# Optimization experiments

Measured on AMD Instinct MI355X. Metric: run time of the kernel, lower is better.

## Reference

```python
import jax, jax.numpy as jnp
import numpy as np

FEATURE_DIM = 128
NUM_EDGES = 640000
NUM_NODES = 40000


def setup_inputs() -> dict:
    key = jax.random.key(0)
    ks = jax.random.split(key, 10)
    d = FEATURE_DIM
    scale = 1.0 / np.sqrt(d)
    inp = {
        "messages": jax.random.normal(ks[0], (NUM_EDGES, d), dtype=jnp.float32),
        "receivers": jax.random.randint(ks[1], (NUM_EDGES,), 0, NUM_NODES, dtype=jnp.int32),
        "num_segments": NUM_NODES,
        "Wk": jax.random.normal(ks[2], (d, d), dtype=jnp.float32) * scale,
        "bk": jnp.zeros((d,), dtype=jnp.float32),
        "Wv": jax.random.normal(ks[3], (d, d), dtype=jnp.float32) * scale,
        "bv": jnp.zeros((d,), dtype=jnp.float32),
        "Wq": jax.random.normal(ks[4], (d, d), dtype=jnp.float32) * scale,
        "bq": jnp.zeros((d,), dtype=jnp.float32),
        "Wo": jax.random.normal(ks[5], (d, d), dtype=jnp.float32) * scale,
        "bo": jnp.zeros((d,), dtype=jnp.float32),
    }
    return inp


def reference(messages, receivers, num_segments, Wk, bk, Wv, bv, Wq, bq, Wo, bo):
    d = messages.shape[-1]
    # per-edge key/value projections
    keys = messages @ Wk + bk            # [E, d]
    values = messages @ Wv + bv          # [E, d]
    # node-level summed messages -> queries
    summed = jax.ops.segment_sum(messages, receivers, num_segments)  # [N, d]
    queries = summed @ Wq + bq                                       # [N, d]
    # scalar attention score per edge (dot over full feature dim)
    msg_q = queries[receivers]                                       # [E, d]
    scores = jnp.sum(msg_q * keys, axis=-1) / jnp.sqrt(jnp.float32(d))  # [E]
    # segment softmax over edges sharing a receiver
    max_s = jax.ops.segment_max(scores, receivers, num_segments)     # [N]
    exp_s = jnp.exp(scores - max_s[receivers])                       # [E]
    sum_e = jax.ops.segment_sum(exp_s, receivers, num_segments)      # [N]
    attn = exp_s / (sum_e[receivers] + 1e-08)                        # [E]
    # weighted scatter-sum of values, then output projection
    agg = jax.ops.segment_sum(values * attn[:, None], receivers, num_segments)  # [N, d]
    return agg @ Wo + bo
```

## Files before the change

kernel.cpp:

```cpp
#include <hip/hip_runtime.h>

#define D 128
#define RSQRT_D 0.088388347648318440550f
#define NEG_HUGE -3.4e38f
#define CAPW 70

#define FMA4(acc, s, b) { acc.x += (s)*(b).x; acc.y += (s)*(b).y; acc.z += (s)*(b).z; acc.w += (s)*(b).w; }

__device__ __forceinline__ void gld_lds16(const void* g, void* l) {
    __builtin_amdgcn_global_load_lds((const __attribute__((address_space(1))) void*)g,
                                     (__attribute__((address_space(3))) void*)l, 16, 0, 0);
}

__global__ __launch_bounds__(256) void prep_kernel(
    const float* __restrict__ Wq, const float* __restrict__ Wk,
    const float* __restrict__ bq, const float* __restrict__ bk,
    const float* __restrict__ Wv, const float* __restrict__ Wo,
    const float* __restrict__ bv,
    float* __restrict__ Wqk, float* __restrict__ bqk,
    float* __restrict__ wqb, float* __restrict__ bqb,
    float* __restrict__ Wvo, float* __restrict__ bvo,
    int* __restrict__ zbase, int zcount) {
    int bid = blockIdx.x, t = threadIdx.x;
    if (bid < 64) {
        int i = bid * 2 + (t >> 7), j = t & 127;
        float a1 = 0.f, a2 = 0.f;
        for (int u = 0; u < D; ++u) {
            a1 += Wq[i * D + u] * Wk[j * D + u];
            a2 += Wv[i * D + u] * Wo[u * D + j];
        }
        Wqk[i * D + j] = a1;
        Wvo[i * D + j] = a2;
    } else if (bid == 64) {
        if (t < D) {
            int j = t;
            float a1 = 0.f, a2 = 0.f, a3 = 0.f;
            for (int u = 0; u < D; ++u) {
                a1 += bq[u] * Wk[j * D + u];
                a2 += Wq[j * D + u] * bk[u];
                a3 += bv[u] * Wo[u * D + j];
            }
            bqk[j] = a1; wqb[j] = a2; bvo[j] = a3;
            if (j == 0) {
                float b = 0.f;
                for (int u = 0; u < D; ++u) b += bq[u] * bk[u];
                *bqb = b;
            }
        }
    } else {
        int idx = (bid - 65) * 256 + t;
        if (idx < zcount) zbase[idx] = 0;
    }
}

__global__ void hist_kernel(const int* __restrict__ recv, int* __restrict__ cnt, int E) {
    int e = blockIdx.x * blockDim.x + threadIdx.x;
    if (e >= E) return;
    atomicAdd(&cnt[recv[e]], 1);
}

__global__ __launch_bounds__(1024) void scan_kernel(const int* __restrict__ cnt,
                                                    int* __restrict__ start, int N) {
    __shared__ int wsum[16];
    __shared__ int chunk_total;
    int t = threadIdx.x;
    int w = t >> 6, lane = t & 63;
    int running = 0;
    const int4* cnt4 = (const int4*)cnt;
    int nIter = (N + 4095) >> 12;
    int4 v = make_int4(0, 0, 0, 0);
    {
        int i = t << 2;
        if (i < N) v = cnt4[i >> 2];
    }
    for (int it = 0; it < nIter; ++it) {
        int4 vn = make_int4(0, 0, 0, 0);
        {
            int i = ((it + 1) << 12) + (t << 2);
            if (it + 1 < nIter && i < N) vn = cnt4[i >> 2];
        }
        int s0 = v.x, s1 = s0 + v.y, s2 = s1 + v.z, s3 = s2 + v.w;
        int x = s3;
#pragma unroll
        for (int off = 1; off < 64; off <<= 1) {
            int y = __shfl_up(x, off);
            if (lane >= off) x += y;
        }
        if (lane == 63) wsum[w] = x;
        __syncthreads();
        if (w == 0 && lane < 16) {
            int s = wsum[lane];
#pragma unroll
            for (int off = 1; off < 16; off <<= 1) {
                int y = __shfl_up(s, off);
                if (lane >= off) s += y;
            }
            wsum[lane] = s;
            if (lane == 15) chunk_total = s;
        }
        __syncthreads();
        int waveoff = (w == 0) ? 0 : wsum[w - 1];
        int tb = running + waveoff + (x - s3);
        int i = (it << 12) + (t << 2);
        if (i < N) ((int4*)start)[i >> 2] = make_int4(tb, tb + s0, tb + s1, tb + s2);
        running += chunk_total;
        __syncthreads();
        v = vn;
    }
    if (t == 0) start[N] = running;
}

__global__ void fill_kernel(const int* __restrict__ recv, const int* __restrict__ start,
                            int* __restrict__ cursor, int* __restrict__ eidx, int E) {
    int e = blockIdx.x * blockDim.x + threadIdx.x;
    if (e >= E) return;
    int r = recv[e];
    int p = atomicAdd(&cursor[r], 1);
    eidx[start[r] + p] = e;
}

__global__ __launch_bounds__(128, 1) void mega_kernel(
    const float* __restrict__ msg, const int* __restrict__ eidx,
    const int* __restrict__ start,
    const float* __restrict__ Wqk, const float* __restrict__ bqk,
    const float* __restrict__ wqb, const float* __restrict__ bqbp,
    const float* __restrict__ Wvo, const float* __restrict__ bvo,
    const float* __restrict__ bo,
    float* __restrict__ out, int N) {
    __shared__ float4 cache4[2 * CAPW * 32];
    __shared__ float4 sums4[8 * 32];
    __shared__ float4 qks4[8 * 32];
    __shared__ float sat[8];

    int t = threadIdx.x;
    int lane = t & 63, w = t >> 6;
    int h = lane >> 5;
    int k = lane & 31;
    int base = blockIdx.x * 8;
    const float4* msg4 = (const float4*)msg;

    int n0 = base + w * 4;
    int sw0 = start[min(n0, N)];
    int sw1 = start[min(n0 + 4, N)];
    int Tw = sw1 - sw0;
    int Tc = min(Tw, CAPW);

    int e0 = (lane < Tc) ? eidx[sw0 + lane] : 0;
    int e1 = (lane + 64 < Tc) ? eidx[sw0 + 64 + lane] : 0;
    float* cbase = (float*)&cache4[w * CAPW * 32];
    int npairs = (Tc + 1) >> 1;
    for (int p = 0; p < npairs; ++p) {
        int row = 2 * p + h;
        int rr = min(row, Tc - 1);
        int e = (rr < 64) ? __shfl(e0, rr) : __shfl(e1, rr - 64);
        gld_lds16(msg + (size_t)e * D + (k << 2), cbase + p * 256);
    }
    asm volatile("s_waitcnt vmcnt(0)" ::: "memory");

    for (int b = 0; b < 4; ++b) {
        int n = n0 + b;
        if (n >= N) break;
        int nl = n - base;
        int q0 = start[n] - sw0, q1 = start[n + 1] - sw0;
        float4 a = make_float4(0.f, 0.f, 0.f, 0.f);
        for (int j = q0; j < q1; j += 2) {
            int row = j + h;
            int rr = min(row, q1 - 1);
            float4 f;
            if (rr < Tc) f = cache4[(w * CAPW + rr) * 32 + k];
            else f = msg4[(size_t)eidx[sw0 + rr] * 32 + k];
            float mk = (row < q1) ? 1.f : 0.f;
            a.x += f.x * mk; a.y += f.y * mk; a.z += f.z * mk; a.w += f.w * mk;
        }
        a.x += __shfl_xor(a.x, 32);
        a.y += __shfl_xor(a.y, 32);
        a.z += __shfl_xor(a.z, 32);
        a.w += __shfl_xor(a.w, 32);
        if (lane < 32) sums4[nl * 32 + k] = a;
    }
    __syncthreads();

    {
        int c = t & 31, slot = t >> 5;
        const float4* B4 = (const float4*)Wqk;
        float4 acc0 = ((const float4*)bqk)[c];
        float4 acc1 = acc0;
        for (int i = 0; i < D; i += 4) {
            float4 aA = sums4[slot * 32 + (i >> 2)];
            float4 aB = sums4[(slot + 4) * 32 + (i >> 2)];
            float4 b0 = B4[(i + 0) * 32 + c];
            float4 b1 = B4[(i + 1) * 32 + c];
            float4 b2 = B4[(i + 2) * 32 + c];
            float4 b3 = B4[(i + 3) * 32 + c];
            FMA4(acc0, aA.x, b0); FMA4(acc0, aA.y, b1); FMA4(acc0, aA.z, b2); FMA4(acc0, aA.w, b3);
            FMA4(acc1, aB.x, b0); FMA4(acc1, aB.y, b1); FMA4(acc1, aB.z, b2); FMA4(acc1, aB.w, b3);
        }
        qks4[slot * 32 + c] = acc0;
        qks4[(slot + 4) * 32 + c] = acc1;
    }
    __syncthreads();

    float bqb = bqbp[0];
    for (int b = 0; b < 4; ++b) {
        int n = n0 + b;
        if (n >= N) break;
        int nl = n - base;
        int q0 = start[n] - sw0, q1 = start[n + 1] - sw0;
        float4 q = qks4[nl * 32 + k];
        float4 sv = sums4[nl * 32 + k];
        float4 wv = ((const float4*)wqb)[k];
        float pq = sv.x * wv.x + sv.y * wv.y + sv.z * wv.z + sv.w * wv.w;
        pq += __shfl_xor(pq, 1); pq += __shfl_xor(pq, 2); pq += __shfl_xor(pq, 4);
        pq += __shfl_xor(pq, 8); pq += __shfl_xor(pq, 16);
        float qb = pq + bqb;

        float m = NEG_HUGE, s = 0.f;
        float4 acc = make_float4(0.f, 0.f, 0.f, 0.f);
        for (int j = q0; j < q1; j += 2) {
            int row = j + h;
            int rr = min(row, q1 - 1);
            float4 f;
            if (rr < Tc) f = cache4[(w * CAPW + rr) * 32 + k];
            else f = msg4[(size_t)eidx[sw0 + rr] * 32 + k];
            int valid = row < q1;
            float p = f.x * q.x + f.y * q.y + f.z * q.z + f.w * q.w;
            p += __shfl_xor(p, 1); p += __shfl_xor(p, 2); p += __shfl_xor(p, 4);
            p += __shfl_xor(p, 8); p += __shfl_xor(p, 16);
            float sc = valid ? (p + qb) * RSQRT_D : NEG_HUGE;
            float nm = fmaxf(m, sc);
            float scale = __expf(m - nm);
            float ww = __expf(sc - nm);
            s = s * scale + ww;
            acc.x = acc.x * scale + ww * f.x;
            acc.y = acc.y * scale + ww * f.y;
            acc.z = acc.z * scale + ww * f.z;
            acc.w = acc.w * scale + ww * f.w;
            m = nm;
        }
        float mo = __shfl_xor(m, 32);
        float so = __shfl_xor(s, 32);
        float4 ao;
        ao.x = __shfl_xor(acc.x, 32); ao.y = __shfl_xor(acc.y, 32);
        ao.z = __shfl_xor(acc.z, 32); ao.w = __shfl_xor(acc.w, 32);
        float mt = fmaxf(m, mo);
        float c0 = __expf(m - mt), c1 = __expf(mo - mt);
        float st = s * c0 + so * c1;
        float4 aT;
        aT.x = acc.x * c0 + ao.x * c1;
        aT.y = acc.y * c0 + ao.y * c1;
        aT.z = acc.z * c0 + ao.z * c1;
        aT.w = acc.w * c0 + ao.w * c1;
        float inv = 1.f / (st + 1e-8f);
        if (lane < 32)
            sums4[nl * 32 + k] = make_float4(aT.x * inv, aT.y * inv, aT.z * inv, aT.w * inv);
        if (lane == 0) sat[nl] = st * inv;
    }
    __syncthreads();

    {
        int c = t & 31, slot = t >> 5;
        const float4* B4 = (const float4*)Wvo;
        float4 bo4 = ((const float4*)bo)[c];
        float4 bv4 = ((const float4*)bvo)[c];
        float sa0 = sat[slot], sa1 = sat[slot + 4];
        float4 acc0 = make_float4(bo4.x + sa0 * bv4.x, bo4.y + sa0 * bv4.y,
                                  bo4.z + sa0 * bv4.z, bo4.w + sa0 * bv4.w);
        float4 acc1 = make_float4(bo4.x + sa1 * bv4.x, bo4.y + sa1 * bv4.y,
                                  bo4.z + sa1 * bv4.z, bo4.w + sa1 * bv4.w);
        for (int i = 0; i < D; i += 4) {
            float4 aA = sums4[slot * 32 + (i >> 2)];
            float4 aB = sums4[(slot + 4) * 32 + (i >> 2)];
            float4 b0 = B4[(i + 0) * 32 + c];
            float4 b1 = B4[(i + 1) * 32 + c];
            float4 b2 = B4[(i + 2) * 32 + c];
            float4 b3 = B4[(i + 3) * 32 + c];
            FMA4(acc0, aA.x, b0); FMA4(acc0, aA.y, b1); FMA4(acc0, aA.z, b2); FMA4(acc0, aA.w, b3);
            FMA4(acc1, aB.x, b0); FMA4(acc1, aB.y, b1); FMA4(acc1, aB.z, b2); FMA4(acc1, aB.w, b3);
        }
        int nA = base + slot, nB = base + slot + 4;
        if (nA < N) ((float4*)(out + (size_t)nA * D))[c] = acc0;
        if (nB < N) ((float4*)(out + (size_t)nB * D))[c] = acc1;
    }
}


extern "C" void kernel_launch(void* const* d_in, const int* in_sizes, int n_in,
                              void* d_out, int out_size, void* d_ws, size_t ws_size,
                              hipStream_t stream) {
    const float* msg = (const float*)d_in[0];
    const int* recv = (const int*)d_in[1];
    const float* Wk = (const float*)d_in[3];
    const float* bk = (const float*)d_in[4];
    const float* Wv = (const float*)d_in[5];
    const float* bv = (const float*)d_in[6];
    const float* Wq = (const float*)d_in[7];
    const float* bq = (const float*)d_in[8];
    const float* Wo = (const float*)d_in[9];
    const float* bo = (const float*)d_in[10];
    float* out = (float*)d_out;

    int E = in_sizes[0] / D;
    int N = out_size / D;

    char* wsb = (char*)d_ws;
    size_t o = 0;
    auto alloc = [&](size_t elems) {
        void* p = wsb + o;
        o += (elems * 4 + 63) & ~(size_t)63;
        return p;
    };

    int* cnt    = (int*)alloc(N);
    int* cursor = (int*)alloc(N);
    int* start  = (int*)alloc(N + 1);
    int* eidx   = (int*)alloc(E);
    float* Wqk  = (float*)alloc(D * D);
    float* bqk  = (float*)alloc(D);
    float* wqb  = (float*)alloc(D);
    float* bqb  = (float*)alloc(1);
    float* Wvo  = (float*)alloc(D * D);
    float* bvo  = (float*)alloc(D);

    int zcount = 2 * N;
    int zblocks = (zcount + 255) / 256;
    prep_kernel<<<65 + zblocks, 256, 0, stream>>>(Wq, Wk, bq, bk, Wv, Wo, bv,
                                                  Wqk, bqk, wqb, bqb, Wvo, bvo,
                                                  cnt, zcount);
    int nbE = (E + 255) / 256;
    hist_kernel<<<nbE, 256, 0, stream>>>(recv, cnt, E);
    scan_kernel<<<1, 1024, 0, stream>>>(cnt, start, N);
    fill_kernel<<<nbE, 256, 0, stream>>>(recv, start, cursor, eidx, E);
    mega_kernel<<<(N + 7) / 8, 128, 0, stream>>>(msg, eidx, start, Wqk, bqk, wqb, bqb,
                                                 Wvo, bvo, bo, out, N);
}
```

Measured before the change: 753.6 us.

## Replace LDS message cache with register-prefetched multi-pass segment softmax

The per-wave LDS cache of message rows, filled with direct global-to-LDS loads, is removed. Each block now handles 16 nodes with 256 threads and stages edge indices in shared memory. Each wave walks all edges of its 4 nodes as one contiguous range with a software-prefetched 8-row register pipeline, in three passes: sum, score/max, then exp-weighted accumulate. Dropping the cache frees LDS and allows 4 blocks per CU, which should give more occupancy and memory parallelism than the single-block, latency-bound design. The cost is reading message rows from global memory three times instead of once, relying on L2 to hold them, plus extra select logic per row.

```diff
diff --git a/kernel.cpp b/kernel.cpp
--- a/kernel.cpp
+++ b/kernel.cpp
@@ -3,14 +3,13 @@
 #define D 128
 #define RSQRT_D 0.088388347648318440550f
 #define NEG_HUGE -3.4e38f
-#define CAPW 70
+#define NPB 16
+#define CAP 512
 
 #define FMA4(acc, s, b) { acc.x += (s)*(b).x; acc.y += (s)*(b).y; acc.z += (s)*(b).z; acc.w += (s)*(b).w; }
-
-__device__ __forceinline__ void gld_lds16(const void* g, void* l) {
-    __builtin_amdgcn_global_load_lds((const __attribute__((address_space(1))) void*)g,
-                                     (__attribute__((address_space(3))) void*)l, 16, 0, 0);
-}
+#define ADD4(acc, b) { acc.x += (b).x; acc.y += (b).y; acc.z += (b).z; acc.w += (b).w; }
+#define MRG4(a) { a.x += __shfl_xor(a.x,32); a.y += __shfl_xor(a.y,32); a.z += __shfl_xor(a.z,32); a.w += __shfl_xor(a.w,32); }
+#define Z4 make_float4(0.f,0.f,0.f,0.f)
 
 __global__ __launch_bounds__(256) void prep_kernel(
     const float* __restrict__ Wq, const float* __restrict__ Wk,
@@ -119,7 +118,14 @@
     eidx[start[r] + p] = e;
 }
 
-__global__ __launch_bounds__(128, 1) void mega_kernel(
+__device__ __forceinline__ float hdot32(float4 f, float4 q) {
+    float p = f.x * q.x + f.y * q.y + f.z * q.z + f.w * q.w;
+    p += __shfl_xor(p, 1); p += __shfl_xor(p, 2); p += __shfl_xor(p, 4);
+    p += __shfl_xor(p, 8); p += __shfl_xor(p, 16);
+    return p;
+}
+
+__global__ __launch_bounds__(256, 4) void mega_kernel(
     const float* __restrict__ msg, const int* __restrict__ eidx,
     const int* __restrict__ start,
     const float* __restrict__ Wqk, const float* __restrict__ bqk,
@@ -127,56 +133,75 @@
     const float* __restrict__ Wvo, const float* __restrict__ bvo,
     const float* __restrict__ bo,
     float* __restrict__ out, int N) {
-    __shared__ float4 cache4[2 * CAPW * 32];
-    __shared__ float4 sums4[8 * 32];
-    __shared__ float4 qks4[8 * 32];
-    __shared__ float sat[8];
+    __shared__ float4 sums4[NPB * 32];
+    __shared__ float4 qks4[NPB * 32];
+    __shared__ int eidx_s[CAP];
+    __shared__ float s_s[CAP];
+    __shared__ float sat[NPB];
 
     int t = threadIdx.x;
     int lane = t & 63, w = t >> 6;
     int h = lane >> 5;
     int k = lane & 31;
-    int base = blockIdx.x * 8;
+    int base = blockIdx.x * NPB;
     const float4* msg4 = (const float4*)msg;
 
+    int nendB = min(base + NPB, N);
+    int s0B = start[base];
+    int cntB = start[nendB] - s0B;
+    int cc = min(cntB, CAP);
+    for (int i = t; i < cc; i += 256) eidx_s[i] = eidx[s0B + i];
+
     int n0 = base + w * 4;
-    int sw0 = start[min(n0, N)];
-    int sw1 = start[min(n0 + 4, N)];
-    int Tw = sw1 - sw0;
-    int Tc = min(Tw, CAPW);
-
-    int e0 = (lane < Tc) ? eidx[sw0 + lane] : 0;
-    int e1 = (lane + 64 < Tc) ? eidx[sw0 + 64 + lane] : 0;
-    float* cbase = (float*)&cache4[w * CAPW * 32];
-    int npairs = (Tc + 1) >> 1;
-    for (int p = 0; p < npairs; ++p) {
-        int row = 2 * p + h;
-        int rr = min(row, Tc - 1);
-        int e = (rr < 64) ? __shfl(e0, rr) : __shfl(e1, rr - 64);
-        gld_lds16(msg + (size_t)e * D + (k << 2), cbase + p * 256);
-    }
-    asm volatile("s_waitcnt vmcnt(0)" ::: "memory");
-
-    for (int b = 0; b < 4; ++b) {
-        int n = n0 + b;
-        if (n >= N) break;
-        int nl = n - base;
-        int q0 = start[n] - sw0, q1 = start[n + 1] - sw0;
-        float4 a = make_float4(0.f, 0.f, 0.f, 0.f);
-        for (int j = q0; j < q1; j += 2) {
-            int row = j + h;
-            int rr = min(row, q1 - 1);
-            float4 f;
-            if (rr < Tc) f = cache4[(w * CAPW + rr) * 32 + k];
-            else f = msg4[(size_t)eidx[sw0 + rr] * 32 + k];
-            float mk = (row < q1) ? 1.f : 0.f;
-            a.x += f.x * mk; a.y += f.y * mk; a.z += f.z * mk; a.w += f.w * mk;
-        }
-        a.x += __shfl_xor(a.x, 32);
-        a.y += __shfl_xor(a.y, 32);
-        a.z += __shfl_xor(a.z, 32);
-        a.w += __shfl_xor(a.w, 32);
-        if (lane < 32) sums4[nl * 32 + k] = a;
+    int b0 = start[min(n0 + 0, N)] - s0B;
+    int b1 = start[min(n0 + 1, N)] - s0B;
+    int b2 = start[min(n0 + 2, N)] - s0B;
+    int b3 = start[min(n0 + 3, N)] - s0B;
+    int b4 = start[min(n0 + 4, N)] - s0B;
+
+    __syncthreads();
+
+    auto loadrow = [&](int r) -> float4 {
+        int rI = min(r, b4 - 1);
+        int e = (rI < CAP) ? eidx_s[rI] : eidx[s0B + rI];
+        return msg4[(size_t)e * 32 + k];
+    };
+
+    float4 a0 = Z4, a1 = Z4, a2 = Z4, a3 = Z4;
+    if (b0 < b4) {
+        int j = b0;
+        float4 F0 = loadrow(j + h), F1 = loadrow(j + h + 2),
+               F2 = loadrow(j + h + 4), F3 = loadrow(j + h + 6);
+        for (;;) {
+            int jn = j + 8;
+            bool more = jn < b4;
+            float4 G0, G1, G2, G3;
+            if (more) {
+                G0 = loadrow(jn + h); G1 = loadrow(jn + h + 2);
+                G2 = loadrow(jn + h + 4); G3 = loadrow(jn + h + 6);
+            }
+#pragma unroll
+            for (int u = 0; u < 4; ++u) {
+                int r = j + h + 2 * u;
+                float4 g = (u == 0) ? F0 : (u == 1) ? F1 : (u == 2) ? F2 : F3;
+                float mk = (r < b4) ? 1.f : 0.f;
+                g.x *= mk; g.y *= mk; g.z *= mk; g.w *= mk;
+                if (r < b1)      { ADD4(a0, g); }
+                else if (r < b2) { ADD4(a1, g); }
+                else if (r < b3) { ADD4(a2, g); }
+                else             { ADD4(a3, g); }
+            }
+            if (!more) break;
+            F0 = G0; F1 = G1; F2 = G2; F3 = G3;
+            j = jn;
+        }
+    }
+    MRG4(a0); MRG4(a1); MRG4(a2); MRG4(a3);
+    if (lane < 32) {
+        sums4[(w * 4 + 0) * 32 + k] = a0;
+        sums4[(w * 4 + 1) * 32 + k] = a1;
+        sums4[(w * 4 + 2) * 32 + k] = a2;
+        sums4[(w * 4 + 3) * 32 + k] = a3;
     }
     __syncthreads();
 
@@ -187,73 +212,132 @@
         float4 acc1 = acc0;
         for (int i = 0; i < D; i += 4) {
             float4 aA = sums4[slot * 32 + (i >> 2)];
-            float4 aB = sums4[(slot + 4) * 32 + (i >> 2)];
-            float4 b0 = B4[(i + 0) * 32 + c];
-            float4 b1 = B4[(i + 1) * 32 + c];
-            float4 b2 = B4[(i + 2) * 32 + c];
-            float4 b3 = B4[(i + 3) * 32 + c];
-            FMA4(acc0, aA.x, b0); FMA4(acc0, aA.y, b1); FMA4(acc0, aA.z, b2); FMA4(acc0, aA.w, b3);
-            FMA4(acc1, aB.x, b0); FMA4(acc1, aB.y, b1); FMA4(acc1, aB.z, b2); FMA4(acc1, aB.w, b3);
+            float4 aB = sums4[(slot + 8) * 32 + (i >> 2)];
+            float4 c0 = B4[(i + 0) * 32 + c];
+            float4 c1 = B4[(i + 1) * 32 + c];
+            float4 c2 = B4[(i + 2) * 32 + c];
+            float4 c3 = B4[(i + 3) * 32 + c];
+            FMA4(acc0, aA.x, c0); FMA4(acc0, aA.y, c1); FMA4(acc0, aA.z, c2); FMA4(acc0, aA.w, c3);
+            FMA4(acc1, aB.x, c0); FMA4(acc1, aB.y, c1); FMA4(acc1, aB.z, c2); FMA4(acc1, aB.w, c3);
         }
         qks4[slot * 32 + c] = acc0;
-        qks4[(slot + 4) * 32 + c] = acc1;
+        qks4[(slot + 8) * 32 + c] = acc1;
     }
     __syncthreads();
 
+    float4 wv = ((const float4*)wqb)[k];
     float bqb = bqbp[0];
-    for (int b = 0; b < 4; ++b) {
-        int n = n0 + b;
-        if (n >= N) break;
-        int nl = n - base;
-        int q0 = start[n] - sw0, q1 = start[n + 1] - sw0;
-        float4 q = qks4[nl * 32 + k];
-        float4 sv = sums4[nl * 32 + k];
-        float4 wv = ((const float4*)wqb)[k];
-        float pq = sv.x * wv.x + sv.y * wv.y + sv.z * wv.z + sv.w * wv.w;
-        pq += __shfl_xor(pq, 1); pq += __shfl_xor(pq, 2); pq += __shfl_xor(pq, 4);
-        pq += __shfl_xor(pq, 8); pq += __shfl_xor(pq, 16);
-        float qb = pq + bqb;
-
-        float m = NEG_HUGE, s = 0.f;
-        float4 acc = make_float4(0.f, 0.f, 0.f, 0.f);
-        for (int j = q0; j < q1; j += 2) {
-            int row = j + h;
-            int rr = min(row, q1 - 1);
-            float4 f;
-            if (rr < Tc) f = cache4[(w * CAPW + rr) * 32 + k];
-            else f = msg4[(size_t)eidx[sw0 + rr] * 32 + k];
-            int valid = row < q1;
-            float p = f.x * q.x + f.y * q.y + f.z * q.z + f.w * q.w;
-            p += __shfl_xor(p, 1); p += __shfl_xor(p, 2); p += __shfl_xor(p, 4);
-            p += __shfl_xor(p, 8); p += __shfl_xor(p, 16);
-            float sc = valid ? (p + qb) * RSQRT_D : NEG_HUGE;
-            float nm = fmaxf(m, sc);
-            float scale = __expf(m - nm);
-            float ww = __expf(sc - nm);
-            s = s * scale + ww;
-            acc.x = acc.x * scale + ww * f.x;
-            acc.y = acc.y * scale + ww * f.y;
-            acc.z = acc.z * scale + ww * f.z;
-            acc.w = acc.w * scale + ww * f.w;
-            m = nm;
-        }
-        float mo = __shfl_xor(m, 32);
-        float so = __shfl_xor(s, 32);
-        float4 ao;
-        ao.x = __shfl_xor(acc.x, 32); ao.y = __shfl_xor(acc.y, 32);
-        ao.z = __shfl_xor(acc.z, 32); ao.w = __shfl_xor(acc.w, 32);
-        float mt = fmaxf(m, mo);
-        float c0 = __expf(m - mt), c1 = __expf(mo - mt);
-        float st = s * c0 + so * c1;
-        float4 aT;
-        aT.x = acc.x * c0 + ao.x * c1;
-        aT.y = acc.y * c0 + ao.y * c1;
-        aT.z = acc.z * c0 + ao.z * c1;
-        aT.w = acc.w * c0 + ao.w * c1;
-        float inv = 1.f / (st + 1e-8f);
-        if (lane < 32)
-            sums4[nl * 32 + k] = make_float4(aT.x * inv, aT.y * inv, aT.z * inv, aT.w * inv);
-        if (lane == 0) sat[nl] = st * inv;
+    float4 sv0 = sums4[(w * 4 + 0) * 32 + k];
+    float4 sv1 = sums4[(w * 4 + 1) * 32 + k];
+    float4 sv2 = sums4[(w * 4 + 2) * 32 + k];
+    float4 sv3 = sums4[(w * 4 + 3) * 32 + k];
+    float qb0 = hdot32(sv0, wv) + bqb;
+    float qb1 = hdot32(sv1, wv) + bqb;
+    float qb2 = hdot32(sv2, wv) + bqb;
+    float qb3 = hdot32(sv3, wv) + bqb;
+    float4 q0 = qks4[(w * 4 + 0) * 32 + k];
+    float4 q1 = qks4[(w * 4 + 1) * 32 + k];
+    float4 q2 = qks4[(w * 4 + 2) * 32 + k];
+    float4 q3 = qks4[(w * 4 + 3) * 32 + k];
+
+    float m0 = NEG_HUGE, m1 = NEG_HUGE, m2 = NEG_HUGE, m3 = NEG_HUGE;
+    if (b0 < b4) {
+        int j = b0;
+        float4 F0 = loadrow(j + h), F1 = loadrow(j + h + 2),
+               F2 = loadrow(j + h + 4), F3 = loadrow(j + h + 6);
+        for (;;) {
+            int jn = j + 8;
+            bool more = jn < b4;
+            float4 G0, G1, G2, G3;
+            if (more) {
+                G0 = loadrow(jn + h); G1 = loadrow(jn + h + 2);
+                G2 = loadrow(jn + h + 4); G3 = loadrow(jn + h + 6);
+            }
+#pragma unroll
+            for (int u = 0; u < 4; ++u) {
+                int r = j + h + 2 * u;
+                bool valid = r < b4;
+                float4 f = (u == 0) ? F0 : (u == 1) ? F1 : (u == 2) ? F2 : F3;
+                float4 qv = (r < b1) ? q0 : (r < b2) ? q1 : (r < b3) ? q2 : q3;
+                float qbv = (r < b1) ? qb0 : (r < b2) ? qb1 : (r < b3) ? qb2 : qb3;
+                float p = hdot32(f, qv);
+                float sc = valid ? (p + qbv) * RSQRT_D : NEG_HUGE;
+                if (r < b1)      m0 = fmaxf(m0, sc);
+                else if (r < b2) m1 = fmaxf(m1, sc);
+                else if (r < b3) m2 = fmaxf(m2, sc);
+                else             m3 = fmaxf(m3, sc);
+                if (k == 0 && valid && r < CAP) s_s[r] = sc;
+            }
+            if (!more) break;
+            F0 = G0; F1 = G1; F2 = G2; F3 = G3;
+            j = jn;
+        }
+    }
+    m0 = fmaxf(m0, __shfl_xor(m0, 32));
+    m1 = fmaxf(m1, __shfl_xor(m1, 32));
+    m2 = fmaxf(m2, __shfl_xor(m2, 32));
+    m3 = fmaxf(m3, __shfl_xor(m3, 32));
+
+    float sm0 = 0.f, sm1 = 0.f, sm2 = 0.f, sm3 = 0.f;
+    float4 c0 = Z4, c1 = Z4, c2 = Z4, c3 = Z4;
+    if (b0 < b4) {
+        int j = b0;
+        float4 F0 = loadrow(j + h), F1 = loadrow(j + h + 2),
+               F2 = loadrow(j + h + 4), F3 = loadrow(j + h + 6);
+        for (;;) {
+            int jn = j + 8;
+            bool more = jn < b4;
+            float4 G0, G1, G2, G3;
+            if (more) {
+                G0 = loadrow(jn + h); G1 = loadrow(jn + h + 2);
+                G2 = loadrow(jn + h + 4); G3 = loadrow(jn + h + 6);
+            }
+#pragma unroll
+            for (int u = 0; u < 4; ++u) {
+                int r = j + h + 2 * u;
+                bool valid = r < b4;
+                float4 f = (u == 0) ? F0 : (u == 1) ? F1 : (u == 2) ? F2 : F3;
+                int rI = min(r, b4 - 1);
+                float sc;
+                if (rI < CAP) {
+                    sc = s_s[rI];
+                } else {
+                    float4 qv = (r < b1) ? q0 : (r < b2) ? q1 : (r < b3) ? q2 : q3;
+                    float qbv = (r < b1) ? qb0 : (r < b2) ? qb1 : (r < b3) ? qb2 : qb3;
+                    sc = (hdot32(f, qv) + qbv) * RSQRT_D;
+                }
+                float msel = (r < b1) ? m0 : (r < b2) ? m1 : (r < b3) ? m2 : m3;
+                float wgt = valid ? __expf(sc - msel) : 0.f;
+                if (r < b1)      { sm0 += wgt; FMA4(c0, wgt, f); }
+                else if (r < b2) { sm1 += wgt; FMA4(c1, wgt, f); }
+                else if (r < b3) { sm2 += wgt; FMA4(c2, wgt, f); }
+                else             { sm3 += wgt; FMA4(c3, wgt, f); }
+            }
+            if (!more) break;
+            F0 = G0; F1 = G1; F2 = G2; F3 = G3;
+            j = jn;
+        }
+    }
+    sm0 += __shfl_xor(sm0, 32);
+    sm1 += __shfl_xor(sm1, 32);
+    sm2 += __shfl_xor(sm2, 32);
+    sm3 += __shfl_xor(sm3, 32);
+    MRG4(c0); MRG4(c1); MRG4(c2); MRG4(c3);
+    float inv0 = 1.f / (sm0 + 1e-8f);
+    float inv1 = 1.f / (sm1 + 1e-8f);
+    float inv2 = 1.f / (sm2 + 1e-8f);
+    float inv3 = 1.f / (sm3 + 1e-8f);
+    if (lane < 32) {
+        sums4[(w * 4 + 0) * 32 + k] = make_float4(c0.x * inv0, c0.y * inv0, c0.z * inv0, c0.w * inv0);
+        sums4[(w * 4 + 1) * 32 + k] = make_float4(c1.x * inv1, c1.y * inv1, c1.z * inv1, c1.w * inv1);
+        sums4[(w * 4 + 2) * 32 + k] = make_float4(c2.x * inv2, c2.y * inv2, c2.z * inv2, c2.w * inv2);
+        sums4[(w * 4 + 3) * 32 + k] = make_float4(c3.x * inv3, c3.y * inv3, c3.z * inv3, c3.w * inv3);
+    }
+    if (lane == 0) {
+        sat[w * 4 + 0] = sm0 * inv0;
+        sat[w * 4 + 1] = sm1 * inv1;
+        sat[w * 4 + 2] = sm2 * inv2;
+        sat[w * 4 + 3] = sm3 * inv3;
     }
     __syncthreads();
 
@@ -262,22 +346,22 @@
         const float4* B4 = (const float4*)Wvo;
         float4 bo4 = ((const float4*)bo)[c];
         float4 bv4 = ((const float4*)bvo)[c];
-        float sa0 = sat[slot], sa1 = sat[slot + 4];
+        float sa0 = sat[slot], sa1 = sat[slot + 8];
         float4 acc0 = make_float4(bo4.x + sa0 * bv4.x, bo4.y + sa0 * bv4.y,
                                   bo4.z + sa0 * bv4.z, bo4.w + sa0 * bv4.w);
         float4 acc1 = make_float4(bo4.x + sa1 * bv4.x, bo4.y + sa1 * bv4.y,
                                   bo4.z + sa1 * bv4.z, bo4.w + sa1 * bv4.w);
         for (int i = 0; i < D; i += 4) {
             float4 aA = sums4[slot * 32 + (i >> 2)];
-            float4 aB = sums4[(slot + 4) * 32 + (i >> 2)];
-            float4 b0 = B4[(i + 0) * 32 + c];
-            float4 b1 = B4[(i + 1) * 32 + c];
-            float4 b2 = B4[(i + 2) * 32 + c];
-            float4 b3 = B4[(i + 3) * 32 + c];
-            FMA4(acc0, aA.x, b0); FMA4(acc0, aA.y, b1); FMA4(acc0, aA.z, b2); FMA4(acc0, aA.w, b3);
-            FMA4(acc1, aB.x, b0); FMA4(acc1, aB.y, b1); FMA4(acc1, aB.z, b2); FMA4(acc1, aB.w, b3);
-        }
-        int nA = base + slot, nB = base + slot + 4;
+            float4 aB = sums4[(slot + 8) * 32 + (i >> 2)];
+            float4 d0 = B4[(i + 0) * 32 + c];
+            float4 d1 = B4[(i + 1) * 32 + c];
+            float4 d2 = B4[(i + 2) * 32 + c];
+            float4 d3 = B4[(i + 3) * 32 + c];
+            FMA4(acc0, aA.x, d0); FMA4(acc0, aA.y, d1); FMA4(acc0, aA.z, d2); FMA4(acc0, aA.w, d3);
+            FMA4(acc1, aB.x, d0); FMA4(acc1, aB.y, d1); FMA4(acc1, aB.z, d2); FMA4(acc1, aB.w, d3);
+        }
+        int nA = base + slot, nB = base + slot + 8;
         if (nA < N) ((float4*)(out + (size_t)nA * D))[c] = acc0;
         if (nB < N) ((float4*)(out + (size_t)nB * D))[c] = acc1;
     }
@@ -310,8 +394,8 @@
         return p;
     };
 
-    int* cnt    = (int*)alloc(N);
-    int* cursor = (int*)alloc(N);
+    int* cnt    = (int*)alloc(2 * (size_t)N);
+    int* cursor = cnt + N;
     int* start  = (int*)alloc(N + 1);
     int* eidx   = (int*)alloc(E);
     float* Wqk  = (float*)alloc(D * D);
@@ -330,6 +414,6 @@
     hist_kernel<<<nbE, 256, 0, stream>>>(recv, cnt, E);
     scan_kernel<<<1, 1024, 0, stream>>>(cnt, start, N);
     fill_kernel<<<nbE, 256, 0, stream>>>(recv, start, cursor, eidx, E);
-    mega_kernel<<<(N + 7) / 8, 128, 0, stream>>>(msg, eidx, start, Wqk, bqk, wqb, bqb,
-                                                 Wvo, bvo, bo, out, N);
-}
+    mega_kernel<<<(N + NPB - 1) / NPB, 256, 0, stream>>>(msg, eidx, start, Wqk, bqk, wqb, bqb,
+                                                         Wvo, bvo, bo, out, N);
+}
```

Result: faster. 724.0 us (-3.9%).
